# Optimization experiments

Hardware: AMD Instinct MI355X
Metric: run time of the kernel (lower is better)

## Reference

```python
import jax, jax.numpy as jnp
import numpy as np
import math

B, H, S, D = 2, 16, 2048, 64
DROP_P = 0.1


def setup_inputs() -> dict:
    key = jax.random.key(0)
    k1, k2 = jax.random.split(key)
    x1 = jax.random.normal(k1, (B, H, S, D), dtype=jnp.float32)  # queries
    x2 = jax.random.normal(k2, (B, H, S, D), dtype=jnp.float32)  # keys == values
    return {"x1": x1, "x2": x2}


def reference(x1, x2):
    # qk = x1 @ x2^T, scaled by 1/sqrt(head_dim)
    inv_scale = math.sqrt(x1.shape[-1])
    scores = jnp.einsum('bhqd,bhkd->bhqk', x1, x2) / inv_scale  # [B,H,S,S]
    probs = jax.nn.softmax(scores, axis=-1)
    # F.dropout(p=0.1) in training mode: deterministic jax mask with fixed key
    keep = jax.random.bernoulli(jax.random.key(42), 1.0 - DROP_P, probs.shape)
    probs = jnp.where(keep, probs / (1.0 - DROP_P), 0.0)
    out = jnp.einsum('bhqk,bhkd->bhqd', probs, x2)  # [B,H,S,D]
    return out
```

## Files before the change

### kernel.cpp

```cpp
#include <hip/hip_runtime.h>
#include <hip/hip_bf16.h>
#include <math.h>

#define BATCH 2
#define NHEAD 16
#define SLEN  2048
#define DH    64
#define WAVES 4
#define QW    16
#define QB    (WAVES*QW)
#define KB    64
#define PSTRIDE 68

typedef __attribute__((ext_vector_type(8))) short bf16x8;
typedef __attribute__((ext_vector_type(4))) float f32x4;

__device__ __forceinline__ unsigned rotl32(unsigned x, unsigned d) {
    return __builtin_amdgcn_alignbit(x, x, 32u - d);
}

__device__ __forceinline__ unsigned threefry_bits(unsigned i) {
    const unsigned k0 = 0u, k1 = 42u;
    const unsigned ks[3] = { k0, k1, k0 ^ k1 ^ 0x1BD11BDAu };
    unsigned x0 = 0u + ks[0];
    unsigned x1 = i  + ks[1];
#pragma unroll
    for (int g = 0; g < 5; ++g) {
        if ((g & 1) == 0) {
            x0 += x1; x1 = rotl32(x1, 13u); x1 ^= x0;
            x0 += x1; x1 = rotl32(x1, 15u); x1 ^= x0;
            x0 += x1; x1 = rotl32(x1, 26u); x1 ^= x0;
            x0 += x1; x1 = rotl32(x1,  6u); x1 ^= x0;
        } else {
            x0 += x1; x1 = rotl32(x1, 17u); x1 ^= x0;
            x0 += x1; x1 = rotl32(x1, 29u); x1 ^= x0;
            x0 += x1; x1 = rotl32(x1, 16u); x1 ^= x0;
            x0 += x1; x1 = rotl32(x1, 24u); x1 ^= x0;
        }
        x0 += ks[(g + 1) % 3];
        x1 += ks[(g + 2) % 3] + (unsigned)(g + 1);
    }
    return x0 ^ x1;
}

__device__ __forceinline__ int keep(unsigned flat) {
    return threefry_bits(flat) < 3865470464u;
}

__device__ __forceinline__ short f2bf(float f) {
    __hip_bfloat16 h = __float2bfloat16(f);
    return *reinterpret_cast<short*>(&h);
}

__global__ __launch_bounds__(256)
void attn_mfma_kernel(const float* __restrict__ Q,
                      const float* __restrict__ KV,
                      float* __restrict__ O) {
    __shared__ bf16x8 s_k[KB * 8];
    __shared__ bf16x8 s_vt[DH * 9];
    __shared__ float s_p[WAVES][QW][PSTRIDE];

    const int tid  = threadIdx.x;
    const int wave = tid >> 6;
    const int lane = tid & 63;
    const int g    = lane >> 4;
    const int lc   = lane & 15;

    const int blk = blockIdx.x;
    const int bh  = blk >> 5;
    const int q0  = (blk & 31) * QB + wave * QW;

    const float* Qb = Q  + ((size_t)bh * SLEN + q0) * DH;
    const float* Kb = KV + (size_t)bh * SLEN * DH;

    const float qscale = 0.125f * 1.4426950408889634f;
    bf16x8 qa[2];
#pragma unroll
    for (int h = 0; h < 2; ++h) {
        const float* qp = Qb + (size_t)lc * DH + 32 * h + g * 8;
        float4 f0 = *(const float4*)qp;
        float4 f1 = *(const float4*)(qp + 4);
        qa[h][0] = f2bf(f0.x * qscale); qa[h][1] = f2bf(f0.y * qscale);
        qa[h][2] = f2bf(f0.z * qscale); qa[h][3] = f2bf(f0.w * qscale);
        qa[h][4] = f2bf(f1.x * qscale); qa[h][5] = f2bf(f1.y * qscale);
        qa[h][6] = f2bf(f1.z * qscale); qa[h][7] = f2bf(f1.w * qscale);
    }

    f32x4 oacc[4];
#pragma unroll
    for (int t = 0; t < 4; ++t) oacc[t] = (f32x4){0.f, 0.f, 0.f, 0.f};
    float m[4] = { -INFINITY, -INFINITY, -INFINITY, -INFINITY };
    float l[4] = { 0.f, 0.f, 0.f, 0.f };

    const unsigned rowbase = ((unsigned)bh * SLEN + (unsigned)(q0 + g * 4)) * SLEN;
    const unsigned fib = rowbase + (unsigned)lc;

    const int kr0 = tid >> 3;
    const int kc0 = tid & 7;
    const int vd  = tid & 63;
    const int vw  = tid >> 6;

    for (int k0 = 0; k0 < SLEN; k0 += KB) {
        __syncthreads();

#pragma unroll
        for (int rr = 0; rr < 2; ++rr) {
            const int row = kr0 + rr * 32;
            const float* src = Kb + (size_t)(k0 + row) * DH + kc0 * 8;
            float4 f0 = *(const float4*)src;
            float4 f1 = *(const float4*)(src + 4);
            bf16x8 v;
            v[0] = f2bf(f0.x); v[1] = f2bf(f0.y);
            v[2] = f2bf(f0.z); v[3] = f2bf(f0.w);
            v[4] = f2bf(f1.x); v[5] = f2bf(f1.y);
            v[6] = f2bf(f1.z); v[7] = f2bf(f1.w);
            s_k[row * 8 + (kc0 ^ (row & 7))] = v;
        }
#pragma unroll
        for (int rr = 0; rr < 2; ++rr) {
            const int w = vw + rr * 4;
            bf16x8 v;
#pragma unroll
            for (int j = 0; j < 8; ++j)
                v[j] = f2bf(Kb[(size_t)(k0 + w * 8 + j) * DH + vd]);
            s_vt[vd * 9 + w] = v;
        }
        __syncthreads();

        f32x4 s[4];
#pragma unroll
        for (int tt = 0; tt < 4; ++tt) {
            bf16x8 kb0 = s_k[(tt * 16 + lc) * 8 + (g       ^ (lc & 7))];
            bf16x8 kb1 = s_k[(tt * 16 + lc) * 8 + ((4 + g) ^ (lc & 7))];
            f32x4 acc = (f32x4){0.f, 0.f, 0.f, 0.f};
            acc = __builtin_amdgcn_mfma_f32_16x16x32_bf16(qa[0], kb0, acc, 0, 0, 0);
            s[tt] = __builtin_amdgcn_mfma_f32_16x16x32_bf16(qa[1], kb1, acc, 0, 0, 0);
        }

#pragma unroll
        for (int i = 0; i < 4; ++i) {
            float a = s[0][i], b = s[1][i], c = s[2][i], d = s[3][i];
            float t = fmaxf(fmaxf(a, b), fmaxf(c, d));
            t = fmaxf(t, __shfl_xor(t, 1));
            t = fmaxf(t, __shfl_xor(t, 2));
            t = fmaxf(t, __shfl_xor(t, 4));
            t = fmaxf(t, __shfl_xor(t, 8));
            if (t > m[i]) {
                float corr = __builtin_amdgcn_exp2f(m[i] - t);
                l[i] *= corr;
                oacc[0][i] *= corr; oacc[1][i] *= corr;
                oacc[2][i] *= corr; oacc[3][i] *= corr;
                m[i] = t;
            }
            float p0 = __builtin_amdgcn_exp2f(a - m[i]);
            float p1 = __builtin_amdgcn_exp2f(b - m[i]);
            float p2 = __builtin_amdgcn_exp2f(c - m[i]);
            float p3 = __builtin_amdgcn_exp2f(d - m[i]);
            float rs = (p0 + p1) + (p2 + p3);
            rs += __shfl_xor(rs, 1);
            rs += __shfl_xor(rs, 2);
            rs += __shfl_xor(rs, 4);
            rs += __shfl_xor(rs, 8);
            l[i] += rs;

            const unsigned fi = fib + (unsigned)i * SLEN + (unsigned)k0;
            if (!keep(fi))       p0 = 0.f;
            if (!keep(fi + 16u)) p1 = 0.f;
            if (!keep(fi + 32u)) p2 = 0.f;
            if (!keep(fi + 48u)) p3 = 0.f;
            float* pr = &s_p[wave][g * 4 + i][0];
            pr[lc]      = p0;
            pr[lc + 16] = p1;
            pr[lc + 32] = p2;
            pr[lc + 48] = p3;
        }

        const float* pp = &s_p[wave][lc][0];
        float4 pf0 = *(const float4*)(pp + g * 8);
        float4 pf1 = *(const float4*)(pp + g * 8 + 4);
        float4 pf2 = *(const float4*)(pp + 32 + g * 8);
        float4 pf3 = *(const float4*)(pp + 32 + g * 8 + 4);
        bf16x8 pa0, pa1;
        pa0[0] = f2bf(pf0.x); pa0[1] = f2bf(pf0.y);
        pa0[2] = f2bf(pf0.z); pa0[3] = f2bf(pf0.w);
        pa0[4] = f2bf(pf1.x); pa0[5] = f2bf(pf1.y);
        pa0[6] = f2bf(pf1.z); pa0[7] = f2bf(pf1.w);
        pa1[0] = f2bf(pf2.x); pa1[1] = f2bf(pf2.y);
        pa1[2] = f2bf(pf2.z); pa1[3] = f2bf(pf2.w);
        pa1[4] = f2bf(pf3.x); pa1[5] = f2bf(pf3.y);
        pa1[6] = f2bf(pf3.z); pa1[7] = f2bf(pf3.w);

#pragma unroll
        for (int t = 0; t < 4; ++t) {
            bf16x8 vb0 = s_vt[(t * 16 + lc) * 9 + g];
            bf16x8 vb1 = s_vt[(t * 16 + lc) * 9 + 4 + g];
            oacc[t] = __builtin_amdgcn_mfma_f32_16x16x32_bf16(pa0, vb0, oacc[t], 0, 0, 0);
            oacc[t] = __builtin_amdgcn_mfma_f32_16x16x32_bf16(pa1, vb1, oacc[t], 0, 0, 0);
        }
    }

#pragma unroll
    for (int i = 0; i < 4; ++i) {
        float sc = 1.0f / (l[i] * 0.9f);
        float* orow = O + ((size_t)bh * SLEN + (size_t)(q0 + g * 4 + i)) * DH;
        orow[lc]      = oacc[0][i] * sc;
        orow[16 + lc] = oacc[1][i] * sc;
        orow[32 + lc] = oacc[2][i] * sc;
        orow[48 + lc] = oacc[3][i] * sc;
    }
}

extern "C" void kernel_launch(void* const* d_in, const int* in_sizes, int n_in,
                              void* d_out, int out_size, void* d_ws, size_t ws_size,
                              hipStream_t stream) {
    const float* x1 = (const float*)d_in[0];
    const float* x2 = (const float*)d_in[1];
    float* out = (float*)d_out;
    const int nblocks = BATCH * NHEAD * (SLEN / QB);
    attn_mfma_kernel<<<dim3(nblocks), dim3(256), 0, stream>>>(x1, x2, out);
}
```

Before: 334.9 us.

## Precompute dropout mask as packed bitmask in a separate kernel

Adds a separate kernel that evaluates the Threefry dropout test for every score element and packs the results into 64-bit words, one bit per element. The attention kernel then loads one word per row per key tile and tests bits instead of running Threefry inline. The aim is to take the heavy integer hashing out of the MFMA/softmax loop so it runs in a simple, fully parallel ALU kernel. The cost is an extra launch and about 16 MB of mask traffic. If the workspace is too small the mask is placed in the output buffer, which only works because each block reads its mask rows before writing the same bytes of output.

```diff
diff --git a/kernel.cpp b/kernel.cpp
--- a/kernel.cpp
+++ b/kernel.cpp
@@ -43,8 +43,18 @@
     return x0 ^ x1;
 }
 
-__device__ __forceinline__ int keep(unsigned flat) {
-    return threefry_bits(flat) < 3865470464u;
+__global__ __launch_bounds__(256)
+void mask_kernel(unsigned long long* __restrict__ M) {
+    const unsigned w = blockIdx.x * 256u + threadIdx.x;
+    const unsigned ebase = ((w >> 5) << 11) | ((w & 31) << 6);
+    unsigned lo = 0u, hi = 0u;
+#pragma unroll 8
+    for (int j = 0; j < 32; ++j)
+        lo |= (threefry_bits(ebase + (unsigned)j) < 3865470464u ? 1u : 0u) << j;
+#pragma unroll 8
+    for (int j = 0; j < 32; ++j)
+        hi |= (threefry_bits(ebase + 32u + (unsigned)j) < 3865470464u ? 1u : 0u) << j;
+    M[w] = ((unsigned long long)hi << 32) | (unsigned long long)lo;
 }
 
 __device__ __forceinline__ short f2bf(float f) {
@@ -55,6 +65,7 @@
 __global__ __launch_bounds__(256)
 void attn_mfma_kernel(const float* __restrict__ Q,
                       const float* __restrict__ KV,
+                      const unsigned long long* M,
                       float* __restrict__ O) {
     __shared__ bf16x8 s_k[KB * 8];
     __shared__ bf16x8 s_vt[DH * 9];
@@ -72,6 +83,11 @@
 
     const float* Qb = Q  + ((size_t)bh * SLEN + q0) * DH;
     const float* Kb = KV + (size_t)bh * SLEN * DH;
+
+    const unsigned long long* mp[4];
+#pragma unroll
+    for (int i = 0; i < 4; ++i)
+        mp[i] = M + ((size_t)bh * SLEN + (size_t)(q0 + g * 4 + i)) * 32;
 
     const float qscale = 0.125f * 1.4426950408889634f;
     bf16x8 qa[2];
@@ -92,15 +108,13 @@
     float m[4] = { -INFINITY, -INFINITY, -INFINITY, -INFINITY };
     float l[4] = { 0.f, 0.f, 0.f, 0.f };
 
-    const unsigned rowbase = ((unsigned)bh * SLEN + (unsigned)(q0 + g * 4)) * SLEN;
-    const unsigned fib = rowbase + (unsigned)lc;
-
     const int kr0 = tid >> 3;
     const int kc0 = tid & 7;
     const int vd  = tid & 63;
     const int vw  = tid >> 6;
 
     for (int k0 = 0; k0 < SLEN; k0 += KB) {
+        const int s = k0 >> 6;
         __syncthreads();
 
 #pragma unroll
@@ -127,19 +141,19 @@
         }
         __syncthreads();
 
-        f32x4 s[4];
+        f32x4 sarr[4];
 #pragma unroll
         for (int tt = 0; tt < 4; ++tt) {
             bf16x8 kb0 = s_k[(tt * 16 + lc) * 8 + (g       ^ (lc & 7))];
             bf16x8 kb1 = s_k[(tt * 16 + lc) * 8 + ((4 + g) ^ (lc & 7))];
             f32x4 acc = (f32x4){0.f, 0.f, 0.f, 0.f};
             acc = __builtin_amdgcn_mfma_f32_16x16x32_bf16(qa[0], kb0, acc, 0, 0, 0);
-            s[tt] = __builtin_amdgcn_mfma_f32_16x16x32_bf16(qa[1], kb1, acc, 0, 0, 0);
+            sarr[tt] = __builtin_amdgcn_mfma_f32_16x16x32_bf16(qa[1], kb1, acc, 0, 0, 0);
         }
 
 #pragma unroll
         for (int i = 0; i < 4; ++i) {
-            float a = s[0][i], b = s[1][i], c = s[2][i], d = s[3][i];
+            float a = sarr[0][i], b = sarr[1][i], c = sarr[2][i], d = sarr[3][i];
             float t = fmaxf(fmaxf(a, b), fmaxf(c, d));
             t = fmaxf(t, __shfl_xor(t, 1));
             t = fmaxf(t, __shfl_xor(t, 2));
@@ -163,11 +177,13 @@
             rs += __shfl_xor(rs, 8);
             l[i] += rs;
 
-            const unsigned fi = fib + (unsigned)i * SLEN + (unsigned)k0;
-            if (!keep(fi))       p0 = 0.f;
-            if (!keep(fi + 16u)) p1 = 0.f;
-            if (!keep(fi + 32u)) p2 = 0.f;
-            if (!keep(fi + 48u)) p3 = 0.f;
+            const unsigned long long mw = mp[i][s];
+            const unsigned mlo = (unsigned)mw;
+            const unsigned mhi = (unsigned)(mw >> 32);
+            if (!((mlo >> lc) & 1u))        p0 = 0.f;
+            if (!((mlo >> (lc + 16)) & 1u)) p1 = 0.f;
+            if (!((mhi >> lc) & 1u))        p2 = 0.f;
+            if (!((mhi >> (lc + 16)) & 1u)) p3 = 0.f;
             float* pr = &s_p[wave][g * 4 + i][0];
             pr[lc]      = p0;
             pr[lc + 16] = p1;
@@ -216,6 +232,14 @@
     const float* x1 = (const float*)d_in[0];
     const float* x2 = (const float*)d_in[1];
     float* out = (float*)d_out;
+
+    const size_t mask_bytes = (size_t)BATCH * NHEAD * SLEN * SLEN / 8;
+    unsigned long long* mask = (ws_size >= mask_bytes)
+        ? (unsigned long long*)d_ws : (unsigned long long*)d_out;
+
+    const int mask_words = (int)(mask_bytes / 8);
+    mask_kernel<<<dim3(mask_words / 256), dim3(256), 0, stream>>>(mask);
+
     const int nblocks = BATCH * NHEAD * (SLEN / QB);
-    attn_mfma_kernel<<<dim3(nblocks), dim3(256), 0, stream>>>(x1, x2, out);
-}
+    attn_mfma_kernel<<<dim3(nblocks), dim3(256), 0, stream>>>(x1, x2, mask, out);
+}
```

New measurement: 419.4 us. 25.2% more time.
